# Kernel tuning notes

Measured on AMD Instinct MI355X. Metric: run time of the kernel, lower is better.

The kernel has to match this reference:

```python
import jax, jax.numpy as jnp
import numpy as np

NUM_HEADS = 4
LN_EPS = 1e-5


def _gcn_layer(src, dst, feats, skip_w, skip_b, msg_w, msg_b):
    # DGL GCNLayer: symmetric degree norm (from src rows), copy_u+sum aggregation,
    # msg linear + affine skip. No activation is applied in the original forward.
    n = feats.shape[0]
    deg = jax.ops.segment_sum(jnp.ones(src.shape, feats.dtype), src, num_segments=n)
    dinv = jnp.where(deg > 0, deg ** -0.5, jnp.zeros_like(deg))
    h = feats * dinv[:, None]                                  # [N, D]
    agg = jax.ops.segment_sum(h[src], dst, num_segments=n)     # scatter-sum over edges
    rst = agg * dinv[:, None]
    return rst @ msg_w.T + msg_b + feats @ skip_w.T + skip_b


def _layernorm(x, g, b):
    mu = jnp.mean(x, axis=-1, keepdims=True)
    var = jnp.mean((x - mu) ** 2, axis=-1, keepdims=True)
    return (x - mu) * jax.lax.rsqrt(var + LN_EPS) * g + b


def _cross_attention(x, seq, in_proj_w, in_proj_b, out_proj_w, out_proj_b, ln_g, ln_b):
    # Unbatched torch nn.MultiheadAttention(query=x [N,D], key=value=seq [S,D]).
    n, d = x.shape
    hd = d // NUM_HEADS
    wq, wk, wv = in_proj_w[:d], in_proj_w[d:2 * d], in_proj_w[2 * d:]
    bq, bk, bv = in_proj_b[:d], in_proj_b[d:2 * d], in_proj_b[2 * d:]
    q = (x @ wq.T + bq).reshape(n, NUM_HEADS, hd)
    k = (seq @ wk.T + bk).reshape(-1, NUM_HEADS, hd)
    v = (seq @ wv.T + bv).reshape(-1, NUM_HEADS, hd)
    scores = jnp.einsum('nhd,shd->hns', q, k) / jnp.sqrt(jnp.asarray(hd, x.dtype))
    attn = jax.nn.softmax(scores, axis=-1)
    o = jnp.einsum('hns,shd->nhd', attn, v).reshape(n, d)
    o = o @ out_proj_w.T + out_proj_b
    # dropout is identity in eval mode; residual + layernorm (num_cross_att == 1 path)
    return _layernorm(o + x, ln_g, ln_b)


def reference(x, seq_embeddings, src, dst, edge_label_index,
              skip_w0, skip_b0, msg_w0, msg_b0,
              skip_w1, skip_b1, msg_w1, msg_b1,
              in_proj_w, in_proj_b, out_proj_w, out_proj_b, ln_g, ln_b,
              weight1, weight2):
    x = _gcn_layer(src, dst, x, skip_w0, skip_b0, msg_w0, msg_b0)
    x = _gcn_layer(src, dst, x, skip_w1, skip_b1, msg_w1, msg_b1)
    x = _cross_attention(x, seq_embeddings, in_proj_w, in_proj_b,
                         out_proj_w, out_proj_b, ln_g, ln_b)
    # F.normalize: row-wise L2
    x = x / jnp.maximum(jnp.linalg.norm(x, axis=-1, keepdims=True), 1e-12)
    node_embedding = x
    p = jax.nn.relu(x @ weight1.T)                # dropout identity (eval)
    p = jax.nn.sigmoid(p @ weight2.T)[:, 0]       # [N]
    # dot edge decoding over last dim of size 1 -> elementwise product
    pred = p[edge_label_index[0]] * p[edge_label_index[1]]
    return pred, node_embedding


def setup_inputs() -> dict:
    key = jax.random.key(0)
    ks = jax.random.split(key, 20)
    N, E, S, D, K = 8192, 524288, 2048, 128, 100000
    s = 1.0 / np.sqrt(D)  # xavier-ish scale for weight matrices
    inp = {
        'x': jax.random.normal(ks[0], (N, D), jnp.float32),
        'seq_embeddings': jax.random.normal(ks[1], (S, D), jnp.float32),
        'src': jax.random.randint(ks[2], (E,), 0, N, jnp.int32),
        'dst': jax.random.randint(ks[3], (E,), 0, N, jnp.int32),
        'edge_label_index': jax.random.randint(ks[4], (2, K), 0, N, jnp.int32),
        'skip_w0': jax.random.normal(ks[5], (D, D), jnp.float32) * s,
        'skip_b0': jnp.zeros((D,), jnp.float32),
        'msg_w0': jax.random.normal(ks[6], (D, D), jnp.float32) * s,
        'msg_b0': jnp.zeros((D,), jnp.float32),
        'skip_w1': jax.random.normal(ks[7], (D, D), jnp.float32) * s,
        'skip_b1': jnp.zeros((D,), jnp.float32),
        'msg_w1': jax.random.normal(ks[8], (D, D), jnp.float32) * s,
        'msg_b1': jnp.zeros((D,), jnp.float32),
        'in_proj_w': jax.random.normal(ks[9], (3 * D, D), jnp.float32) * s,
        'in_proj_b': jnp.zeros((3 * D,), jnp.float32),
        'out_proj_w': jax.random.normal(ks[10], (D, D), jnp.float32) * s,
        'out_proj_b': jnp.zeros((D,), jnp.float32),
        'ln_g': jnp.ones((D,), jnp.float32),
        'ln_b': jnp.zeros((D,), jnp.float32),
        'weight1': jax.random.normal(ks[11], (D, D), jnp.float32) * s,
        'weight2': jax.random.normal(ks[12], (1, D), jnp.float32) * s,
    }
    return inp
```

## Files before the change

kernel.cpp:

```cpp
#include <hip/hip_runtime.h>
#include <math.h>

#define D 128
#define HB 128
#define FA_PS 88
#define SPLITS 4

typedef short bf16x4 __attribute__((ext_vector_type(4)));
typedef short bf16x8 __attribute__((ext_vector_type(8)));
typedef float f32x4 __attribute__((ext_vector_type(4)));

__device__ __forceinline__ float4 ld4(const float* p) { return *(const float4*)p; }

__device__ __forceinline__ short f2bf_r(float f) {
  return (short)((__float_as_uint(f) + 0x8000u) >> 16);
}
__device__ __forceinline__ float bf2f(short s) {
  return __uint_as_float(((unsigned)(unsigned short)s) << 16);
}
__device__ __forceinline__ unsigned pack_bf2(float a, float b) {
  unsigned ua = __float_as_uint(a) + 0x8000u;
  unsigned ub = __float_as_uint(b) + 0x8000u;
  return __builtin_amdgcn_perm(ub, ua, 0x07060302);
}

struct WSrc { const float* p[9]; };
__global__ __launch_bounds__(256) void prep_hist_kernel(
    WSrc ws, short* __restrict__ Wbf,
    const float* __restrict__ x, short* __restrict__ xbf, int* __restrict__ MkhI,
    const int* __restrict__ src, const int* __restrict__ dst,
    unsigned short* __restrict__ histd, unsigned short* __restrict__ hists,
    int E, int NB_COPY) {
  __shared__ int hd[8192];
  __shared__ int hs[8192];
  int b = blockIdx.x, t = threadIdx.x;
  if (b < NB_COPY) {
    if (b == 0 && t < 4) MkhI[t] = 0;
    if (b < 144) {
      int m = b >> 4, blk = b & 15;
      int i = (blk * 256 + t) * 4;
      float4 v = ld4(ws.p[m] + i);
      bf16x4 o = {f2bf_r(v.x), f2bf_r(v.y), f2bf_r(v.z), f2bf_r(v.w)};
      *(bf16x4*)&Wbf[m * 16384 + i] = o;
    } else {
      int i = ((b - 144) * 256 + t) * 4;
      float4 v = ld4(x + i);
      bf16x4 o = {f2bf_r(v.x), f2bf_r(v.y), f2bf_r(v.z), f2bf_r(v.w)};
      *(bf16x4*)&xbf[i] = o;
    }
    return;
  }
  int hb = b - NB_COPY;
  for (int i = t; i < 8192; i += 256) { hd[i] = 0; hs[i] = 0; }
  __syncthreads();
  int per = E / HB;
  int b0 = hb * per;
  for (int j = 0; j < per; j += 256) {
    int i = b0 + j + t;
    atomicAdd(&hd[dst[i]], 1);
    atomicAdd(&hs[src[i]], 1);
  }
  __syncthreads();
  for (int i = t; i < 8192; i += 256) {
    histd[hb * 8192 + i] = (unsigned short)hd[i];
    hists[hb * 8192 + i] = (unsigned short)hs[i];
  }
}

__global__ __launch_bounds__(256) void colsum_kernel(
    const unsigned short* __restrict__ histd, const unsigned short* __restrict__ hists,
    int* __restrict__ deg, float* __restrict__ dinv) {
  int v = blockIdx.x * 256 + threadIdx.x;
  int sd = 0, ss = 0;
  for (int b = 0; b < HB; ++b) { sd += histd[b * 8192 + v]; ss += hists[b * 8192 + v]; }
  deg[v] = sd;
  dinv[v] = ss > 0 ? rsqrtf((float)ss) : 0.f;
}

__global__ __launch_bounds__(1024) void scan8k_kernel(
    const int* __restrict__ deg, int* __restrict__ row_ptr, int N) {
  __shared__ int wtot[16];
  int t = threadIdx.x;
  int lane = t & 63, wv = t >> 6;
  int v0 = t * 8;
  int x[8]; int s = 0;
#pragma unroll
  for (int j = 0; j < 8; ++j) { x[j] = s; s += deg[v0 + j]; }
  int incl = s;
  for (int off = 1; off < 64; off <<= 1) {
    int y = __shfl_up(incl, off);
    if (lane >= off) incl += y;
  }
  if (lane == 63) wtot[wv] = incl;
  __syncthreads();
  if (t == 0) { int run = 0; for (int i = 0; i < 16; ++i) { int v = wtot[i]; wtot[i] = run; run += v; } }
  __syncthreads();
  int base = wtot[wv] + (incl - s);
#pragma unroll
  for (int j = 0; j < 8; ++j) row_ptr[v0 + j] = base + x[j];
  if (t == 1023) row_ptr[N] = base + s;
}

__global__ __launch_bounds__(256) void basegen_kernel(
    const unsigned short* __restrict__ histd, const int* __restrict__ row_ptr,
    int* __restrict__ base_arr) {
  int v = blockIdx.x * 256 + threadIdx.x;
  int run = row_ptr[v];
  for (int b = 0; b < HB; ++b) { base_arr[b * 8192 + v] = run; run += histd[b * 8192 + v]; }
}

__global__ __launch_bounds__(256) void scatter2_kernel(
    const int* __restrict__ src, const int* __restrict__ dst,
    const int* __restrict__ base_arr, int* __restrict__ csr_src, int E) {
  __shared__ int lh[8192];
  int t = threadIdx.x;
  for (int i = t; i < 8192; i += 256) lh[i] = 0;
  __syncthreads();
  int per = E / HB;
  int b0 = blockIdx.x * per;
  const int* __restrict__ bb = &base_arr[blockIdx.x * 8192];
  for (int j = 0; j < per; j += 256) {
    int i = b0 + j + t;
    int v = dst[i];
    int r = atomicAdd(&lh[v], 1);
    csr_src[bb[v] + r] = src[i];
  }
}

__global__ __launch_bounds__(128) void agg_kernel(
    const short* __restrict__ fbf, const float* __restrict__ dinv,
    const int* __restrict__ row_ptr, const int* __restrict__ csr_src,
    short* __restrict__ outbf) {
  __shared__ int idx[128];
  __shared__ float dv[128];
  __shared__ float red[8][128];
  int n = blockIdx.x, t = threadIdx.x;
  int grp = t >> 4, l16 = t & 15;
  int beg = row_ptr[n], end = row_ptr[n + 1];
  float a0[8] = {}, a1[8] = {}, a2[8] = {}, a3[8] = {};
  for (int c = beg; c < end; c += 128) {
    int j = c + t;
    if (j < end) { int s = csr_src[j]; idx[t] = s; dv[t] = dinv[s]; }
    __syncthreads();
    int cnt = min(128, end - c);
    int e = grp;
    for (; e + 24 < cnt; e += 32) {
      bf16x8 w0 = *(const bf16x8*)&fbf[(size_t)idx[e] * D + l16 * 8];
      bf16x8 w1 = *(const bf16x8*)&fbf[(size_t)idx[e + 8] * D + l16 * 8];
      bf16x8 w2 = *(const bf16x8*)&fbf[(size_t)idx[e + 16] * D + l16 * 8];
      bf16x8 w3 = *(const bf16x8*)&fbf[(size_t)idx[e + 24] * D + l16 * 8];
      float wt0 = dv[e], wt1 = dv[e + 8], wt2 = dv[e + 16], wt3 = dv[e + 24];
#pragma unroll
      for (int k = 0; k < 8; ++k) {
        a0[k] += bf2f(w0[k]) * wt0;
        a1[k] += bf2f(w1[k]) * wt1;
        a2[k] += bf2f(w2[k]) * wt2;
        a3[k] += bf2f(w3[k]) * wt3;
      }
    }
    for (; e < cnt; e += 8) {
      bf16x8 w0 = *(const bf16x8*)&fbf[(size_t)idx[e] * D + l16 * 8];
      float wt0 = dv[e];
#pragma unroll
      for (int k = 0; k < 8; ++k) a0[k] += bf2f(w0[k]) * wt0;
    }
    __syncthreads();
  }
#pragma unroll
  for (int k = 0; k < 8; ++k) a0[k] += a1[k] + a2[k] + a3[k];
  *(float4*)&red[grp][l16 * 8] = *(float4*)&a0[0];
  *(float4*)&red[grp][l16 * 8 + 4] = *(float4*)&a0[4];
  __syncthreads();
  if (t < 32) {
    int d0 = t * 4;
    float o[4] = {};
#pragma unroll
    for (int g = 0; g < 8; ++g) {
      o[0] += red[g][d0]; o[1] += red[g][d0 + 1];
      o[2] += red[g][d0 + 2]; o[3] += red[g][d0 + 3];
    }
    float w = dinv[n];
    bf16x4 ov = {f2bf_r(o[0] * w), f2bf_r(o[1] * w), f2bf_r(o[2] * w), f2bf_r(o[3] * w)};
    *(bf16x4*)&outbf[(size_t)n * D + d0] = ov;
  }
}

__device__ __forceinline__ void mfma_accum(const short* As, const short* __restrict__ W,
                                           int rt, int ch, int quad, int r16, f32x4* acc) {
#pragma unroll
  for (int ks = 0; ks < 4; ++ks) {
    bf16x8 af = *(bf16x8*)&As[(rt * 16 + r16) * 136 + ks * 32 + quad * 8];
#pragma unroll
    for (int nt = 0; nt < 4; ++nt) {
      bf16x8 bw = *(const bf16x8*)&W[(size_t)(ch * 64 + nt * 16 + r16) * D + ks * 32 + quad * 8];
      acc[nt] = __builtin_amdgcn_mfma_f32_16x16x32_bf16(af, bw, acc[nt], 0, 0, 0);
    }
  }
}

__device__ __forceinline__ void stage_A_f32(const float* __restrict__ A, int m0, short* As) {
  int row = threadIdx.x >> 3, seg = threadIdx.x & 7;
  const float* ap = &A[(size_t)(m0 + row) * D + seg * 16];
  float4 v0 = ld4(ap), v1 = ld4(ap + 4), v2 = ld4(ap + 8), v3 = ld4(ap + 12);
  bf16x8 w0 = {f2bf_r(v0.x), f2bf_r(v0.y), f2bf_r(v0.z), f2bf_r(v0.w),
               f2bf_r(v1.x), f2bf_r(v1.y), f2bf_r(v1.z), f2bf_r(v1.w)};
  bf16x8 w1 = {f2bf_r(v2.x), f2bf_r(v2.y), f2bf_r(v2.z), f2bf_r(v2.w),
               f2bf_r(v3.x), f2bf_r(v3.y), f2bf_r(v3.z), f2bf_r(v3.w)};
  *(bf16x8*)&As[row * 136 + seg * 16] = w0;
  *(bf16x8*)&As[row * 136 + seg * 16 + 8] = w1;
}

__device__ __forceinline__ void stage_A_bf16(const short* __restrict__ A, int m0, short* As) {
  int row = threadIdx.x >> 3, seg = threadIdx.x & 7;
  const short* ap = &A[(size_t)(m0 + row) * D + seg * 16];
  bf16x8 a0 = *(const bf16x8*)ap;
  bf16x8 a1 = *(const bf16x8*)(ap + 8);
  *(bf16x8*)&As[row * 136 + seg * 16] = a0;
  *(bf16x8*)&As[row * 136 + seg * 16 + 8] = a1;
}

__global__ __launch_bounds__(256) void gemm_gcn_kernel(
    const short* __restrict__ A1, const short* __restrict__ W1, const float* __restrict__ b1,
    const short* __restrict__ A2, const short* __restrict__ W2, const float* __restrict__ b2,
    short* __restrict__ Cbf) {
  __shared__ short As[32 * 136];
  const int t = threadIdx.x;
  const int m0 = blockIdx.x * 32;
  const int w = t >> 6, lane = t & 63, quad = lane >> 4, r16 = lane & 15;
  const int rt = w & 1, ch = w >> 1;
  f32x4 acc[4];
  f32x4 zz = {0.f, 0.f, 0.f, 0.f};
  acc[0] = zz; acc[1] = zz; acc[2] = zz; acc[3] = zz;
  stage_A_bf16(A1, m0, As);
  __syncthreads();
  mfma_accum(As, W1, rt, ch, quad, r16, acc);
  __syncthreads();
  stage_A_bf16(A2, m0, As);
  __syncthreads();
  mfma_accum(As, W2, rt, ch, quad, r16, acc);
#pragma unroll
  for (int nt = 0; nt < 4; ++nt) {
    int col = ch * 64 + nt * 16 + r16;
    float bias = b1[col] + b2[col];
#pragma unroll
    for (int g = 0; g < 4; ++g) {
      int row = m0 + rt * 16 + quad * 4 + g;
      Cbf[(size_t)row * D + col] = f2bf_r(acc[nt][g] + bias);
    }
  }
}

__global__ __launch_bounds__(256) void gemm_gcn2q_kernel(
    const short* __restrict__ A1, const short* __restrict__ Wmsg, const float* __restrict__ bmsg,
    const short* __restrict__ B1bf, const short* __restrict__ Wskip, const float* __restrict__ bskip,
    const short* __restrict__ Wq, const float* __restrict__ ipb,
    float* __restrict__ B2, short* __restrict__ Qh, float* __restrict__ qn, int N) {
  __shared__ short As[32 * 136];
  const int t = threadIdx.x;
  const int m0 = blockIdx.x * 32;
  const int w = t >> 6, lane = t & 63, quad = lane >> 4, r16 = lane & 15;
  const int rt = w & 1, ch = w >> 1;
  f32x4 acc[4];
  f32x4 zz = {0.f, 0.f, 0.f, 0.f};
  acc[0] = zz; acc[1] = zz; acc[2] = zz; acc[3] = zz;
  stage_A_bf16(A1, m0, As);
  __syncthreads();
  mfma_accum(As, Wmsg, rt, ch, quad, r16, acc);
  __syncthreads();
  stage_A_bf16(B1bf, m0, As);
  __syncthreads();
  mfma_accum(As, Wskip, rt, ch, quad, r16, acc);
  __syncthreads();
#pragma unroll
  for (int nt = 0; nt < 4; ++nt) {
    int col = ch * 64 + nt * 16 + r16;
    float bias = bmsg[col] + bskip[col];
#pragma unroll
    for (int g = 0; g < 4; ++g) {
      int lr = rt * 16 + quad * 4 + g;
      float v = acc[nt][g] + bias;
      B2[(size_t)(m0 + lr) * D + col] = v;
      As[lr * 136 + col] = f2bf_r(v);
    }
  }
  __syncthreads();
  f32x4 qa[4];
  qa[0] = zz; qa[1] = zz; qa[2] = zz; qa[3] = zz;
  mfma_accum(As, Wq, rt, ch, quad, r16, qa);
  const float SC = 0.25503473f;
  float pq[4][2] = {};
#pragma unroll
  for (int nt = 0; nt < 4; ++nt) {
    int col = ch * 64 + nt * 16 + r16;
    int hq = col >> 5, dq = col & 31;
    float bias = ipb[col];
    int p = nt >> 1;
#pragma unroll
    for (int g = 0; g < 4; ++g) {
      int row = m0 + rt * 16 + quad * 4 + g;
      float vs = (qa[nt][g] + bias) * SC;
      Qh[((size_t)hq * N + row) * 32 + dq] = f2bf_r(vs);
      pq[g][p] += vs * vs;
    }
  }
#pragma unroll
  for (int mask = 1; mask < 16; mask <<= 1)
#pragma unroll
    for (int g = 0; g < 4; ++g) {
      pq[g][0] += __shfl_xor(pq[g][0], mask);
      pq[g][1] += __shfl_xor(pq[g][1], mask);
    }
  if (r16 == 0) {
#pragma unroll
    for (int g = 0; g < 4; ++g) {
      int row = m0 + rt * 16 + quad * 4 + g;
      qn[(ch * 2 + 0) * N + row] = sqrtf(pq[g][0]);
      qn[(ch * 2 + 1) * N + row] = sqrtf(pq[g][1]);
    }
  }
}

__global__ __launch_bounds__(256) void kv_kernel(
    const float* __restrict__ seq,
    const short* __restrict__ Wk, const short* __restrict__ Wv,
    const float* __restrict__ ipb,
    short* __restrict__ Kh, int* __restrict__ MkhI,
    short* __restrict__ Vt, int S) {
  __shared__ short As[32 * 136];
  __shared__ int lmax[4];
  const int t = threadIdx.x;
  const int b = blockIdx.x;
  const int w = t >> 6, lane = t & 63, quad = lane >> 4, r16 = lane & 15;
  const int rt = w & 1, ch = w >> 1;
  if (t < 4) lmax[t] = 0;
  f32x4 acc[4];
  f32x4 zz = {0.f, 0.f, 0.f, 0.f};
  acc[0] = zz; acc[1] = zz; acc[2] = zz; acc[3] = zz;

  if (b < 64) {
    int m0 = b * 32;
    stage_A_f32(seq, m0, As);
    __syncthreads();
    mfma_accum(As, Wk, rt, ch, quad, r16, acc);
    float pk[4][2] = {};
#pragma unroll
    for (int nt = 0; nt < 4; ++nt) {
      int col = ch * 64 + nt * 16 + r16;
      int hk = col >> 5, dk = col & 31;
      float bias = ipb[128 + col];
      int p = nt >> 1;
#pragma unroll
      for (int g = 0; g < 4; ++g) {
        int key = m0 + rt * 16 + quad * 4 + g;
        float v = acc[nt][g] + bias;
        Kh[((size_t)hk * S + key) * 32 + dk] = f2bf_r(v);
        pk[g][p] += v * v;
      }
    }
#pragma unroll
    for (int mask = 1; mask < 16; mask <<= 1)
#pragma unroll
      for (int g = 0; g < 4; ++g) {
        pk[g][0] += __shfl_xor(pk[g][0], mask);
        pk[g][1] += __shfl_xor(pk[g][1], mask);
      }
    if (r16 == 0) {
#pragma unroll
      for (int g = 0; g < 4; ++g) {
        atomicMax(&lmax[ch * 2 + 0], __float_as_int(pk[g][0]));
        atomicMax(&lmax[ch * 2 + 1], __float_as_int(pk[g][1]));
      }
    }
    __syncthreads();
    if (t < 4) atomicMax(&MkhI[t], lmax[t]);
  } else {
    int m0 = (b - 64) * 32;
    stage_A_f32(seq, m0, As);
    __syncthreads();
    mfma_accum(As, Wv, rt, ch, quad, r16, acc);
#pragma unroll
    for (int nt = 0; nt < 4; ++nt) {
      int dim = ch * 64 + nt * 16 + r16;
      float bias = ipb[256 + dim];
#pragma unroll
      for (int g = 0; g < 4; ++g) {
        int s = m0 + rt * 16 + quad * 4 + g;
        int local = s & 63;
        int kp = (local & 15) * 4 + (local >> 4);
        int gcol = (s & ~63) + kp;
        Vt[(size_t)dim * S + gcol] = f2bf_r(acc[nt][g] + bias);
      }
    }
  }
}

__global__ __launch_bounds__(128, 8) void flash_kernel(
    const short* __restrict__ Qh, const short* __restrict__ Kh, const short* __restrict__ Vt,
    const float* __restrict__ qn, const int* __restrict__ MkhI,
    float* __restrict__ Osp, float* __restrict__ lbuf, int N, int S) {
  __shared__ short Ps[2][32 * FA_PS];
  const int wv = threadIdx.x >> 6;
  const int lane = threadIdx.x & 63;
  const int quad = lane >> 4, r16 = lane & 15;
  const int n0 = (blockIdx.x * 2 + wv) * 32;
  const int h = blockIdx.y;
  const int sp = blockIdx.z;
  float* O = Osp + (size_t)sp * N * D;
  const short* Kb = Kh + (size_t)h * S * 32;
  const short* Qb = Qh + (size_t)h * N * 32;
  short* Pw = Ps[wv];

  bf16x8 aq[2];
  aq[0] = *(const bf16x8*)&Qb[(size_t)(n0 + r16) * 32 + quad * 8];
  aq[1] = *(const bf16x8*)&Qb[(size_t)(n0 + 16 + r16) * 32 + quad * 8];

  float sqm = sqrtf(fmaxf(__int_as_float(MkhI[h]), 0.f));
  float msh[2][4];
#pragma unroll
  for (int rt = 0; rt < 2; ++rt)
#pragma unroll
    for (int g = 0; g < 4; ++g)
      msh[rt][g] = fminf(qn[h * N + n0 + rt * 16 + quad * 4 + g] * sqm, 57.7f);

  f32x4 o[2][2], lac[2];
  f32x4 zz = {0.f, 0.f, 0.f, 0.f};
  o[0][0] = zz; o[0][1] = zz; o[1][0] = zz; o[1][1] = zz;
  lac[0] = zz; lac[1] = zz;
  bf16x8 ones = {(short)0x3F80, (short)0x3F80, (short)0x3F80, (short)0x3F80,
                 (short)0x3F80, (short)0x3F80, (short)0x3F80, (short)0x3F80};

  const int span = S / SPLITS;
  const int c0 = sp * span;
  for (int c = c0; c < c0 + span; c += 64) {
    f32x4 s[2][4];
#pragma unroll
    for (int kt = 0; kt < 4; ++kt) {
      bf16x8 bk = *(const bf16x8*)&Kb[(size_t)(c + kt * 16 + r16) * 32 + quad * 8];
      f32x4 z = {0.f, 0.f, 0.f, 0.f};
      s[0][kt] = __builtin_amdgcn_mfma_f32_16x16x32_bf16(aq[0], bk, z, 0, 0, 0);
      s[1][kt] = __builtin_amdgcn_mfma_f32_16x16x32_bf16(aq[1], bk, z, 0, 0, 0);
    }
#pragma unroll
    for (int rt = 0; rt < 2; ++rt)
#pragma unroll
      for (int g = 0; g < 4; ++g) {
        float m = msh[rt][g];
        float p0 = exp2f(s[rt][0][g] - m);
        float p1 = exp2f(s[rt][1][g] - m);
        float p2 = exp2f(s[rt][2][g] - m);
        float p3 = exp2f(s[rt][3][g] - m);
        uint2 uv = {pack_bf2(p0, p1), pack_bf2(p2, p3)};
        *(uint2*)&Pw[(rt * 16 + quad * 4 + g) * FA_PS + r16 * 4] = uv;
      }
    bf16x8 bv[2][2];
#pragma unroll
    for (int kc = 0; kc < 2; ++kc)
#pragma unroll
      for (int nt = 0; nt < 2; ++nt)
        bv[kc][nt] = *(const bf16x8*)&Vt[(size_t)(h * 32 + nt * 16 + r16) * S + c + kc * 32 + quad * 8];
#pragma unroll
    for (int rt = 0; rt < 2; ++rt)
#pragma unroll
      for (int kc = 0; kc < 2; ++kc) {
        bf16x8 ap = *(bf16x8*)&Pw[(rt * 16 + r16) * FA_PS + kc * 32 + quad * 8];
        lac[rt] = __builtin_amdgcn_mfma_f32_16x16x32_bf16(ap, ones, lac[rt], 0, 0, 0);
#pragma unroll
        for (int nt = 0; nt < 2; ++nt)
          o[rt][nt] = __builtin_amdgcn_mfma_f32_16x16x32_bf16(ap, bv[kc][nt], o[rt][nt], 0, 0, 0);
      }
  }
#pragma unroll
  for (int rt = 0; rt < 2; ++rt)
#pragma unroll
    for (int g = 0; g < 4; ++g) {
      int row = n0 + rt * 16 + quad * 4 + g;
#pragma unroll
      for (int nt = 0; nt < 2; ++nt)
        O[(size_t)row * D + h * 32 + nt * 16 + r16] = o[rt][nt][g];
      if (r16 == 0) lbuf[(sp * 4 + h) * N + row] = lac[rt][g];
    }
}

__global__ __launch_bounds__(256) void gemm_op_mlp_kernel(
    const float* __restrict__ Osp, const float* __restrict__ lbuf,
    const short* __restrict__ W, const float* __restrict__ bias,
    const float* __restrict__ Rres, const float* __restrict__ ln_g,
    const float* __restrict__ ln_b, float* __restrict__ emb,
    const short* __restrict__ Wm1, const float* __restrict__ w2,
    float* __restrict__ pbuf, int N) {
  __shared__ short As[32 * 136];
  __shared__ float Cs[32 * 132];
  __shared__ float part[32][2];
  const int t = threadIdx.x;
  const int m0 = blockIdx.x * 32;
  const int w = t >> 6, lane = t & 63, quad = lane >> 4, r16 = lane & 15;
  const int rt = w & 1, ch = w >> 1;
  {
    int row = t >> 3, seg = t & 7;
    int grow = m0 + row;
    int hh = seg >> 1;
    float l = 0.f;
#pragma unroll
    for (int s = 0; s < SPLITS; ++s) l += lbuf[(s * 4 + hh) * N + grow];
    float inv = 1.f / l;
    const float* p = &Osp[(size_t)grow * D + seg * 16];
    size_t st = (size_t)N * D;
    float a16[16] = {};
#pragma unroll
    for (int s = 0; s < SPLITS; ++s) {
#pragma unroll
      for (int q = 0; q < 4; ++q) {
        float4 a = ld4(p + s * st + q * 4);
        a16[q * 4 + 0] += a.x; a16[q * 4 + 1] += a.y;
        a16[q * 4 + 2] += a.z; a16[q * 4 + 3] += a.w;
      }
    }
#pragma unroll
    for (int k = 0; k < 16; ++k) a16[k] *= inv;
    bf16x8 w0 = {f2bf_r(a16[0]), f2bf_r(a16[1]), f2bf_r(a16[2]), f2bf_r(a16[3]),
                 f2bf_r(a16[4]), f2bf_r(a16[5]), f2bf_r(a16[6]), f2bf_r(a16[7])};
    bf16x8 w1 = {f2bf_r(a16[8]), f2bf_r(a16[9]), f2bf_r(a16[10]), f2bf_r(a16[11]),
                 f2bf_r(a16[12]), f2bf_r(a16[13]), f2bf_r(a16[14]), f2bf_r(a16[15])};
    *(bf16x8*)&As[row * 136 + seg * 16] = w0;
    *(bf16x8*)&As[row * 136 + seg * 16 + 8] = w1;
  }
  __syncthreads();
  f32x4 acc[4];
  f32x4 zz = {0.f, 0.f, 0.f, 0.f};
  acc[0] = zz; acc[1] = zz; acc[2] = zz; acc[3] = zz;
  mfma_accum(As, W, rt, ch, quad, r16, acc);
#pragma unroll
  for (int nt = 0; nt < 4; ++nt) {
    int col = ch * 64 + nt * 16 + r16;
    float bs = bias[col];
#pragma unroll
    for (int g = 0; g < 4; ++g) {
      int lr = rt * 16 + quad * 4 + g;
      Cs[lr * 132 + col] = acc[nt][g] + bs + Rres[(size_t)(m0 + lr) * D + col];
    }
  }
  __syncthreads();
  {
    int row = t >> 3, seg = t & 7;
    float xv[16];
#pragma unroll
    for (int q = 0; q < 4; ++q) {
      f32x4 v = *(f32x4*)&Cs[row * 132 + seg * 16 + q * 4];
      xv[q * 4] = v[0]; xv[q * 4 + 1] = v[1]; xv[q * 4 + 2] = v[2]; xv[q * 4 + 3] = v[3];
    }
    float s = 0.f, sq = 0.f;
#pragma unroll
    for (int k = 0; k < 16; ++k) { s += xv[k]; sq += xv[k] * xv[k]; }
#pragma unroll
    for (int mask = 1; mask < 8; mask <<= 1) { s += __shfl_xor(s, mask); sq += __shfl_xor(sq, mask); }
    float mu = s * (1.f / 128.f);
    float var = fmaxf(sq * (1.f / 128.f) - mu * mu, 0.f);
    float rs = rsqrtf(var + 1e-5f);
    float yv[16], nn = 0.f;
#pragma unroll
    for (int q = 0; q < 4; ++q) {
      float4 gg = ld4(&ln_g[seg * 16 + q * 4]);
      float4 bb = ld4(&ln_b[seg * 16 + q * 4]);
      float y0 = (xv[q * 4] - mu) * rs * gg.x + bb.x;
      float y1 = (xv[q * 4 + 1] - mu) * rs * gg.y + bb.y;
      float y2 = (xv[q * 4 + 2] - mu) * rs * gg.z + bb.z;
      float y3 = (xv[q * 4 + 3] - mu) * rs * gg.w + bb.w;
      yv[q * 4] = y0; yv[q * 4 + 1] = y1; yv[q * 4 + 2] = y2; yv[q * 4 + 3] = y3;
      nn += y0 * y0 + y1 * y1 + y2 * y2 + y3 * y3;
    }
#pragma unroll
    for (int mask = 1; mask < 8; mask <<= 1) nn += __shfl_xor(nn, mask);
    float inv = 1.f / fmaxf(sqrtf(nn), 1e-12f);
    float ev[16];
#pragma unroll
    for (int k = 0; k < 16; ++k) ev[k] = yv[k] * inv;
#pragma unroll
    for (int q = 0; q < 4; ++q) {
      float4 ov = {ev[q * 4], ev[q * 4 + 1], ev[q * 4 + 2], ev[q * 4 + 3]};
      *(float4*)&emb[(size_t)(m0 + row) * D + seg * 16 + q * 4] = ov;
    }
    bf16x8 e0 = {f2bf_r(ev[0]), f2bf_r(ev[1]), f2bf_r(ev[2]), f2bf_r(ev[3]),
                 f2bf_r(ev[4]), f2bf_r(ev[5]), f2bf_r(ev[6]), f2bf_r(ev[7])};
    bf16x8 e1 = {f2bf_r(ev[8]), f2bf_r(ev[9]), f2bf_r(ev[10]), f2bf_r(ev[11]),
                 f2bf_r(ev[12]), f2bf_r(ev[13]), f2bf_r(ev[14]), f2bf_r(ev[15])};
    *(bf16x8*)&As[row * 136 + seg * 16] = e0;
    *(bf16x8*)&As[row * 136 + seg * 16 + 8] = e1;
  }
  __syncthreads();
  f32x4 ma[4];
  ma[0] = zz; ma[1] = zz; ma[2] = zz; ma[3] = zz;
  mfma_accum(As, Wm1, rt, ch, quad, r16, ma);
  float pg[4] = {};
#pragma unroll
  for (int nt = 0; nt < 4; ++nt) {
    float wv2 = w2[ch * 64 + nt * 16 + r16];
#pragma unroll
    for (int g = 0; g < 4; ++g) pg[g] += fmaxf(ma[nt][g], 0.f) * wv2;
  }
#pragma unroll
  for (int mask = 1; mask < 16; mask <<= 1)
#pragma unroll
    for (int g = 0; g < 4; ++g) pg[g] += __shfl_xor(pg[g], mask);
  if (r16 == 0) {
#pragma unroll
    for (int g = 0; g < 4; ++g) part[rt * 16 + quad * 4 + g][ch] = pg[g];
  }
  __syncthreads();
  if (t < 32) {
    float sv = part[t][0] + part[t][1];
    pbuf[m0 + t] = 1.f / (1.f + __expf(-sv));
  }
}

__global__ void pred_kernel(const float* __restrict__ p, const int* __restrict__ eli,
                            float* __restrict__ out, int K) {
  int i = blockIdx.x * blockDim.x + threadIdx.x;
  if (i < K) out[i] = p[eli[i]] * p[eli[K + i]];
}

extern "C" void kernel_launch(void* const* d_in, const int* in_sizes, int n_in,
                              void* d_out, int out_size, void* d_ws, size_t ws_size,
                              hipStream_t stream) {
  const float* x       = (const float*)d_in[0];
  const float* seq     = (const float*)d_in[1];
  const int* src       = (const int*)d_in[2];
  const int* dst       = (const int*)d_in[3];
  const int* eli       = (const int*)d_in[4];
  const float* skip_w0 = (const float*)d_in[5];
  const float* skip_b0 = (const float*)d_in[6];
  const float* msg_w0  = (const float*)d_in[7];
  const float* msg_b0  = (const float*)d_in[8];
  const float* skip_w1 = (const float*)d_in[9];
  const float* skip_b1 = (const float*)d_in[10];
  const float* msg_w1  = (const float*)d_in[11];
  const float* msg_b1  = (const float*)d_in[12];
  const float* ipw     = (const float*)d_in[13];
  const float* ipb     = (const float*)d_in[14];
  const float* opw     = (const float*)d_in[15];
  const float* opb     = (const float*)d_in[16];
  const float* ln_g    = (const float*)d_in[17];
  const float* ln_b    = (const float*)d_in[18];
  const float* w1      = (const float*)d_in[19];
  const float* w2      = (const float*)d_in[20];

  const int N  = in_sizes[0] / D;
  const int S  = in_sizes[1] / D;
  const int E  = in_sizes[2];
  const int Kp = in_sizes[4] / 2;

  float* ws    = (float*)d_ws;
  float* B2    = ws;
  float* Osp   = B2 + (size_t)N * D;
  short* xbf   = (short*)(Osp + (size_t)SPLITS * N * D);
  short* Abf   = xbf + (size_t)N * D;
  short* B1bf  = Abf + (size_t)N * D;
  short* Qh    = B1bf + (size_t)N * D;
  short* Kh    = Qh + (size_t)N * D;
  short* Vt    = Kh + (size_t)S * D;
  short* Wbf   = Vt + (size_t)D * S;
  float* qn    = (float*)(Wbf + 9 * 16384);
  float* lbuf  = qn + 4 * (size_t)N;
  float* dinv  = lbuf + 4 * (size_t)SPLITS * N;
  float* pbuf  = dinv + N;
  int*   MkhI  = (int*)(pbuf + N);
  int*   deg   = MkhI + 4;
  int* row_ptr = deg + N;
  int* csr_src = row_ptr + (N + 1);
  int* base_arr= csr_src + E;
  unsigned short* histd = (unsigned short*)(base_arr + HB * 8192);
  unsigned short* hists = histd + HB * 8192;

  float* pred_out = (float*)d_out;
  float* emb_out  = pred_out + Kp;

  const short* w_skip0 = Wbf + 0 * 16384;
  const short* w_msg0  = Wbf + 1 * 16384;
  const short* w_skip1 = Wbf + 2 * 16384;
  const short* w_msg1  = Wbf + 3 * 16384;
  const short* w_q     = Wbf + 4 * 16384;
  const short* w_k     = Wbf + 5 * 16384;
  const short* w_v     = Wbf + 6 * 16384;
  const short* w_op    = Wbf + 7 * 16384;
  const short* w_m1    = Wbf + 8 * 16384;

  WSrc wsrc;
  wsrc.p[0] = skip_w0; wsrc.p[1] = msg_w0; wsrc.p[2] = skip_w1; wsrc.p[3] = msg_w1;
  wsrc.p[4] = ipw; wsrc.p[5] = ipw + D * D; wsrc.p[6] = ipw + 2 * D * D;
  wsrc.p[7] = opw; wsrc.p[8] = w1;

  const int NB_COPY = 144 + (N * D / 1024);
  prep_hist_kernel<<<NB_COPY + HB, 256, 0, stream>>>(
      wsrc, (short*)Wbf, x, xbf, MkhI, src, dst, histd, hists, E, NB_COPY);

  colsum_kernel<<<N / 256, 256, 0, stream>>>(histd, hists, deg, dinv);
  scan8k_kernel<<<1, 1024, 0, stream>>>(deg, row_ptr, N);
  basegen_kernel<<<N / 256, 256, 0, stream>>>(histd, row_ptr, base_arr);
  scatter2_kernel<<<HB, 256, 0, stream>>>(src, dst, base_arr, csr_src, E);

  agg_kernel<<<N, 128, 0, stream>>>(xbf, dinv, row_ptr, csr_src, Abf);
  gemm_gcn_kernel<<<N / 32, 256, 0, stream>>>(Abf, w_msg0, msg_b0, xbf, w_skip0, skip_b0, B1bf);
  agg_kernel<<<N, 128, 0, stream>>>(B1bf, dinv, row_ptr, csr_src, Abf);
  gemm_gcn2q_kernel<<<N / 32, 256, 0, stream>>>(Abf, w_msg1, msg_b1, B1bf, w_skip1, skip_b1,
                                                w_q, ipb, B2, Qh, qn, N);

  kv_kernel<<<128, 256, 0, stream>>>(seq, w_k, w_v, ipb, Kh, MkhI, Vt, S);

  dim3 fgrid(N / 64, 4, SPLITS);
  flash_kernel<<<fgrid, 128, 0, stream>>>(Qh, Kh, Vt, qn, MkhI, Osp, lbuf, N, S);

  gemm_op_mlp_kernel<<<N / 32, 256, 0, stream>>>(Osp, lbuf, w_op, opb, B2, ln_g, ln_b,
                                                 emb_out, w_m1, w2, pbuf, N);
  pred_kernel<<<(Kp + 255) / 256, 256, 0, stream>>>(pbuf, eli, pred_out, Kp);
}
```

Before: 240.7 us.

## Prefetch next K/V tiles in flash loop and pack two nodes per agg block

The flash attention loop now loads the next chunk's K and V fragments into registers before the softmax and PV MFMAs of the current chunk run, so global load latency overlaps with compute. Its launch bound minimum is lowered from 8 to 4 blocks per CU to leave room for the extra registers. The aggregation kernel now handles two destination nodes per 256-thread block, running rounds set by the larger degree of the pair, which halves the block count. The trade-offs are more register pressure and possibly lower occupancy in flash, and idle threads in agg when the two paired nodes have uneven degrees.

```diff
diff --git a/kernel.cpp b/kernel.cpp
--- a/kernel.cpp
+++ b/kernel.cpp
@@ -127,29 +127,35 @@
   }
 }
 
-__global__ __launch_bounds__(128) void agg_kernel(
+__global__ __launch_bounds__(256) void agg_kernel(
     const short* __restrict__ fbf, const float* __restrict__ dinv,
     const int* __restrict__ row_ptr, const int* __restrict__ csr_src,
     short* __restrict__ outbf) {
-  __shared__ int idx[128];
-  __shared__ float dv[128];
-  __shared__ float red[8][128];
-  int n = blockIdx.x, t = threadIdx.x;
+  __shared__ int idx[2][128];
+  __shared__ float dv[2][128];
+  __shared__ float red[2][8][128];
+  int half = threadIdx.x >> 7, t = threadIdx.x & 127;
+  int nb = blockIdx.x * 2;
+  int n = nb + half;
   int grp = t >> 4, l16 = t & 15;
-  int beg = row_ptr[n], end = row_ptr[n + 1];
+  int r0 = row_ptr[nb], r1 = row_ptr[nb + 1], r2 = row_ptr[nb + 2];
+  int beg = half ? r1 : r0;
+  int end = half ? r2 : r1;
+  int rounds = (max(r1 - r0, r2 - r1) + 127) >> 7;
   float a0[8] = {}, a1[8] = {}, a2[8] = {}, a3[8] = {};
-  for (int c = beg; c < end; c += 128) {
+  for (int r = 0; r < rounds; ++r) {
+    int c = beg + r * 128;
     int j = c + t;
-    if (j < end) { int s = csr_src[j]; idx[t] = s; dv[t] = dinv[s]; }
+    if (j < end) { int s = csr_src[j]; idx[half][t] = s; dv[half][t] = dinv[s]; }
     __syncthreads();
     int cnt = min(128, end - c);
     int e = grp;
     for (; e + 24 < cnt; e += 32) {
-      bf16x8 w0 = *(const bf16x8*)&fbf[(size_t)idx[e] * D + l16 * 8];
-      bf16x8 w1 = *(const bf16x8*)&fbf[(size_t)idx[e + 8] * D + l16 * 8];
-      bf16x8 w2 = *(const bf16x8*)&fbf[(size_t)idx[e + 16] * D + l16 * 8];
-      bf16x8 w3 = *(const bf16x8*)&fbf[(size_t)idx[e + 24] * D + l16 * 8];
-      float wt0 = dv[e], wt1 = dv[e + 8], wt2 = dv[e + 16], wt3 = dv[e + 24];
+      bf16x8 w0 = *(const bf16x8*)&fbf[(size_t)idx[half][e] * D + l16 * 8];
+      bf16x8 w1 = *(const bf16x8*)&fbf[(size_t)idx[half][e + 8] * D + l16 * 8];
+      bf16x8 w2 = *(const bf16x8*)&fbf[(size_t)idx[half][e + 16] * D + l16 * 8];
+      bf16x8 w3 = *(const bf16x8*)&fbf[(size_t)idx[half][e + 24] * D + l16 * 8];
+      float wt0 = dv[half][e], wt1 = dv[half][e + 8], wt2 = dv[half][e + 16], wt3 = dv[half][e + 24];
 #pragma unroll
       for (int k = 0; k < 8; ++k) {
         a0[k] += bf2f(w0[k]) * wt0;
@@ -159,8 +165,8 @@
       }
     }
     for (; e < cnt; e += 8) {
-      bf16x8 w0 = *(const bf16x8*)&fbf[(size_t)idx[e] * D + l16 * 8];
-      float wt0 = dv[e];
+      bf16x8 w0 = *(const bf16x8*)&fbf[(size_t)idx[half][e] * D + l16 * 8];
+      float wt0 = dv[half][e];
 #pragma unroll
       for (int k = 0; k < 8; ++k) a0[k] += bf2f(w0[k]) * wt0;
     }
@@ -168,16 +174,16 @@
   }
 #pragma unroll
   for (int k = 0; k < 8; ++k) a0[k] += a1[k] + a2[k] + a3[k];
-  *(float4*)&red[grp][l16 * 8] = *(float4*)&a0[0];
-  *(float4*)&red[grp][l16 * 8 + 4] = *(float4*)&a0[4];
+  *(float4*)&red[half][grp][l16 * 8] = *(float4*)&a0[0];
+  *(float4*)&red[half][grp][l16 * 8 + 4] = *(float4*)&a0[4];
   __syncthreads();
   if (t < 32) {
     int d0 = t * 4;
     float o[4] = {};
 #pragma unroll
     for (int g = 0; g < 8; ++g) {
-      o[0] += red[g][d0]; o[1] += red[g][d0 + 1];
-      o[2] += red[g][d0 + 2]; o[3] += red[g][d0 + 3];
+      o[0] += red[half][g][d0]; o[1] += red[half][g][d0 + 1];
+      o[2] += red[half][g][d0 + 2]; o[3] += red[half][g][d0 + 3];
     }
     float w = dinv[n];
     bf16x4 ov = {f2bf_r(o[0] * w), f2bf_r(o[1] * w), f2bf_r(o[2] * w), f2bf_r(o[3] * w)};
@@ -394,7 +400,7 @@
   }
 }
 
-__global__ __launch_bounds__(128, 8) void flash_kernel(
+__global__ __launch_bounds__(128, 4) void flash_kernel(
     const short* __restrict__ Qh, const short* __restrict__ Kh, const short* __restrict__ Vt,
     const float* __restrict__ qn, const int* __restrict__ MkhI,
     float* __restrict__ Osp, float* __restrict__ lbuf, int N, int S) {
@@ -431,15 +437,36 @@
 
   const int span = S / SPLITS;
   const int c0 = sp * span;
-  for (int c = c0; c < c0 + span; c += 64) {
+  const int cend = c0 + span;
+
+  bf16x8 bk[4], bv[2][2];
+#pragma unroll
+  for (int kt = 0; kt < 4; ++kt)
+    bk[kt] = *(const bf16x8*)&Kb[(size_t)(c0 + kt * 16 + r16) * 32 + quad * 8];
+#pragma unroll
+  for (int kc = 0; kc < 2; ++kc)
+#pragma unroll
+    for (int nt = 0; nt < 2; ++nt)
+      bv[kc][nt] = *(const bf16x8*)&Vt[(size_t)(h * 32 + nt * 16 + r16) * S + c0 + kc * 32 + quad * 8];
+
+  for (int c = c0; c < cend; c += 64) {
     f32x4 s[2][4];
 #pragma unroll
     for (int kt = 0; kt < 4; ++kt) {
-      bf16x8 bk = *(const bf16x8*)&Kb[(size_t)(c + kt * 16 + r16) * 32 + quad * 8];
       f32x4 z = {0.f, 0.f, 0.f, 0.f};
-      s[0][kt] = __builtin_amdgcn_mfma_f32_16x16x32_bf16(aq[0], bk, z, 0, 0, 0);
-      s[1][kt] = __builtin_amdgcn_mfma_f32_16x16x32_bf16(aq[1], bk, z, 0, 0, 0);
-    }
+      s[0][kt] = __builtin_amdgcn_mfma_f32_16x16x32_bf16(aq[0], bk[kt], z, 0, 0, 0);
+      s[1][kt] = __builtin_amdgcn_mfma_f32_16x16x32_bf16(aq[1], bk[kt], z, 0, 0, 0);
+    }
+    int cn = (c + 64 < cend) ? (c + 64) : c;
+    bf16x8 nk[4], nv[2][2];
+#pragma unroll
+    for (int kt = 0; kt < 4; ++kt)
+      nk[kt] = *(const bf16x8*)&Kb[(size_t)(cn + kt * 16 + r16) * 32 + quad * 8];
+#pragma unroll
+    for (int kc = 0; kc < 2; ++kc)
+#pragma unroll
+      for (int nt = 0; nt < 2; ++nt)
+        nv[kc][nt] = *(const bf16x8*)&Vt[(size_t)(h * 32 + nt * 16 + r16) * S + cn + kc * 32 + quad * 8];
 #pragma unroll
     for (int rt = 0; rt < 2; ++rt)
 #pragma unroll
@@ -452,12 +479,6 @@
         uint2 uv = {pack_bf2(p0, p1), pack_bf2(p2, p3)};
         *(uint2*)&Pw[(rt * 16 + quad * 4 + g) * FA_PS + r16 * 4] = uv;
       }
-    bf16x8 bv[2][2];
-#pragma unroll
-    for (int kc = 0; kc < 2; ++kc)
-#pragma unroll
-      for (int nt = 0; nt < 2; ++nt)
-        bv[kc][nt] = *(const bf16x8*)&Vt[(size_t)(h * 32 + nt * 16 + r16) * S + c + kc * 32 + quad * 8];
 #pragma unroll
     for (int rt = 0; rt < 2; ++rt)
 #pragma unroll
@@ -468,6 +489,12 @@
         for (int nt = 0; nt < 2; ++nt)
           o[rt][nt] = __builtin_amdgcn_mfma_f32_16x16x32_bf16(ap, bv[kc][nt], o[rt][nt], 0, 0, 0);
       }
+#pragma unroll
+    for (int kt = 0; kt < 4; ++kt) bk[kt] = nk[kt];
+#pragma unroll
+    for (int kc = 0; kc < 2; ++kc)
+#pragma unroll
+      for (int nt = 0; nt < 2; ++nt) bv[kc][nt] = nv[kc][nt];
   }
 #pragma unroll
   for (int rt = 0; rt < 2; ++rt)
@@ -697,9 +724,9 @@
   basegen_kernel<<<N / 256, 256, 0, stream>>>(histd, row_ptr, base_arr);
   scatter2_kernel<<<HB, 256, 0, stream>>>(src, dst, base_arr, csr_src, E);
 
-  agg_kernel<<<N, 128, 0, stream>>>(xbf, dinv, row_ptr, csr_src, Abf);
+  agg_kernel<<<N / 2, 256, 0, stream>>>(xbf, dinv, row_ptr, csr_src, Abf);
   gemm_gcn_kernel<<<N / 32, 256, 0, stream>>>(Abf, w_msg0, msg_b0, xbf, w_skip0, skip_b0, B1bf);
-  agg_kernel<<<N, 128, 0, stream>>>(B1bf, dinv, row_ptr, csr_src, Abf);
+  agg_kernel<<<N / 2, 256, 0, stream>>>(B1bf, dinv, row_ptr, csr_src, Abf);
   gemm_gcn2q_kernel<<<N / 32, 256, 0, stream>>>(Abf, w_msg1, msg_b1, B1bf, w_skip1, skip_b1,
                                                 w_q, ipb, B2, Qh, qn, N);
 
```

Measured after the change: 239.7 us. No clear change (-0.4%).
